# Performance work log

Hardware: AMD Instinct MI355X
Metric: run time of the kernel (lower is better)

The kernel has to match this reference:

```python
import jax, jax.numpy as jnp
import numpy as np

EPS = 1e-5
N_GRAPHS = 64


def gcn_conv(x, W, b, src, dst, n_nodes):
    # GCNConv: out = D^{-1/2} (A + I) D^{-1/2} X W + b
    xw = x @ W  # [N, H]
    # add self loops
    loops = jnp.arange(n_nodes, dtype=src.dtype)
    src_f = jnp.concatenate([src, loops])
    dst_f = jnp.concatenate([dst, loops])
    deg = jax.ops.segment_sum(jnp.ones_like(dst_f, dtype=xw.dtype), dst_f, num_segments=n_nodes)
    dinv = jnp.where(deg > 0, jax.lax.rsqrt(deg), 0.0)
    norm = dinv[src_f] * dinv[dst_f]  # [E+N]
    msg = xw[src_f] * norm[:, None]  # gather + scale
    out = jax.ops.segment_sum(msg, dst_f, num_segments=n_nodes)  # scatter-add
    return out + b


def batchnorm(x):
    # fresh BatchNorm1d in training mode: identity affine, batch stats, biased var
    mean = jnp.mean(x, axis=0)
    var = jnp.mean((x - mean) ** 2, axis=0)
    return (x - mean) * jax.lax.rsqrt(var + EPS)


def setup_inputs() -> dict:
    key = jax.random.key(0)
    ks = jax.random.split(key, 12)
    N, E, F, H, C = 65536, 1048576, 64, 64, 16
    x = jax.random.normal(ks[0], (N, F), dtype=jnp.float32)
    edge_index = jax.random.randint(ks[1], (2, E), 0, N, dtype=jnp.int64)
    batch = jnp.sort(jax.random.randint(ks[2], (N,), 0, N_GRAPHS, dtype=jnp.int64))
    s = 1.0 / np.sqrt(H)
    W0 = jax.random.normal(ks[3], (F, H), dtype=jnp.float32) * s
    b0 = jax.random.normal(ks[4], (H,), dtype=jnp.float32) * 0.1
    W1 = jax.random.normal(ks[5], (H, H), dtype=jnp.float32) * s
    b1 = jax.random.normal(ks[6], (H,), dtype=jnp.float32) * 0.1
    W2 = jax.random.normal(ks[7], (H, H), dtype=jnp.float32) * s
    b2 = jax.random.normal(ks[8], (H,), dtype=jnp.float32) * 0.1
    clf_W = jax.random.normal(ks[9], (C, H), dtype=jnp.float32) * s
    clf_b = jax.random.normal(ks[10], (C,), dtype=jnp.float32) * 0.1
    return {"x": x, "edge_index": edge_index, "batch": batch,
            "W0": W0, "b0": b0, "W1": W1, "b1": b1, "W2": W2, "b2": b2,
            "clf_W": clf_W, "clf_b": clf_b}


def reference(x, edge_index, batch, W0, b0, W1, b1, W2, b2, clf_W, clf_b):
    n_nodes = x.shape[0]
    src, dst = edge_index[0], edge_index[1]
    weights = [(W0, b0), (W1, b1), (W2, b2)]
    n_conv = len(weights)
    h = x
    for i, (W, b) in enumerate(weights):
        h = gcn_conv(h, W, b, src, dst, n_nodes)
        if i < n_conv - 1:
            h = jax.nn.relu(h)
        h = batchnorm(h)
    # global mean pool over graphs
    sums = jax.ops.segment_sum(h, batch, num_segments=N_GRAPHS)
    cnts = jax.ops.segment_sum(jnp.ones((n_nodes,), h.dtype), batch, num_segments=N_GRAPHS)
    pooled = sums / jnp.maximum(cnts, 1.0)[:, None]
    logits = pooled @ clf_W.T + clf_b
    return jax.nn.softmax(logits, axis=1)
```

## Files before the change

### kernel.cpp

```cpp
#include <hip/hip_runtime.h>
#include <hip/hip_fp16.h>


#define NBKT 512
#define CAP  4096
#define BSTRIDE 16
#define NSLOT 16
#define GSL   2048

__device__ inline unsigned pack2h(float a, float b) {
    __half ha = __float2half_rn(a), hb = __float2half_rn(b);
    unsigned short ua = *(unsigned short*)&ha, ub = *(unsigned short*)&hb;
    return (unsigned)ua | ((unsigned)ub << 16);
}

__device__ inline void acc8(float* a, uint4 u) {
    __half2* hp = (__half2*)&u;
#pragma unroll
    for (int i = 0; i < 4; ++i) {
        float2 f = __half22float2(hp[i]);
        a[2 * i] += f.x;
        a[2 * i + 1] += f.y;
    }
}

__global__ void k_binit(int* __restrict__ bcur, float* __restrict__ gstats,
                        float* __restrict__ psum, float* __restrict__ pcnt) {
    int idx = blockIdx.x * 256 + threadIdx.x;
    if (idx < NBKT) bcur[idx * BSTRIDE] = idx * CAP;
    for (int i = idx; i < 3 * NSLOT * GSL; i += 32768) gstats[i] = 0.0f;
    if (idx < 4096) psum[idx] = 0.0f;
    if (idx < 64) pcnt[idx] = 0.0f;
}

__global__ void k_bin(const int* __restrict__ ei, int E, int* __restrict__ bcur,
                      int* __restrict__ buck) {
    __shared__ int sd[4096];
    __shared__ unsigned short bk[4096];
    __shared__ int cnt[NBKT], off[NBKT];
    int t = threadIdx.x;
    int base = blockIdx.x * 4096;
    for (int i = t; i < NBKT; i += 256) cnt[i] = 0;
    __syncthreads();
#pragma unroll
    for (int k = 0; k < 16; ++k) {
        int i = k * 256 + t;
        int e = base + i;
        int s = ei[e], d = ei[E + e];
        sd[i] = (s << 7) | (d & 127);
        int b = d >> 7;
        bk[i] = (unsigned short)b;
        atomicAdd(&cnt[b], 1);
    }
    __syncthreads();
    for (int b = t; b < NBKT; b += 256) {
        int c = cnt[b];
        off[b] = c ? atomicAdd(&bcur[b * BSTRIDE], c) : 0;
    }
    __syncthreads();
#pragma unroll
    for (int k = 0; k < 16; ++k) {
        int i = k * 256 + t;
        int b = bk[i];
        int p = atomicAdd(&off[b], 1);
        buck[p] = sd[i];
    }
}

__global__ void k_scanB(const int* __restrict__ bcur, int* __restrict__ bbase,
                        int* __restrict__ rowptr, int N, int E) {
    __shared__ int s[NBKT];
    int t = threadIdx.x;
    int v = bcur[t * BSTRIDE] - t * CAP;
    s[t] = v;
    __syncthreads();
    for (int o = 1; o < NBKT; o <<= 1) {
        int x = (t >= o) ? s[t - o] : 0;
        __syncthreads();
        s[t] += x;
        __syncthreads();
    }
    bbase[t] = s[t] - v;
    if (t == 0) rowptr[N] = E;
}

__global__ void k_place(const int* __restrict__ bcur, const int* __restrict__ buck,
                        const int* __restrict__ bbase, int* __restrict__ rowptr,
                        float* __restrict__ dinv, int* __restrict__ csr) {
    __shared__ int dc[128], sc[128], cur[128];
    int b = blockIdx.x, t = threadIdx.x;
    if (t < 128) dc[t] = 0;
    __syncthreads();
    int beg = b * CAP, end = bcur[b * BSTRIDE];
    for (int i = beg + t; i < end; i += 256) atomicAdd(&dc[buck[i] & 127], 1);
    __syncthreads();
    int v = (t < 128) ? dc[t] : 0;
    if (t < 128) sc[t] = v;
    __syncthreads();
    for (int o = 1; o < 128; o <<= 1) {
        int x = 0;
        if (t < 128 && t >= o) x = sc[t - o];
        __syncthreads();
        if (t < 128) sc[t] += x;
        __syncthreads();
    }
    if (t < 128) {
        int r = bbase[b] + sc[t] - v;
        rowptr[b * 128 + t] = r;
        cur[t] = r;
        dinv[b * 128 + t] = rsqrtf((float)(v + 1));
    }
    __syncthreads();
    for (int i = beg + t; i < end; i += 256) {
        int e = buck[i];
        int p = atomicAdd(&cur[e & 127], 1);
        csr[p] = e >> 7;
    }
}

template <int HIN, int HS>
__global__ void k_gemm(const void* __restrict__ hv, const float* __restrict__ W,
                       const float* __restrict__ gstats, float invN,
                       const float* __restrict__ dinv, __half* __restrict__ y) {
    __shared__ float Ws[4096];
    __shared__ float hs[64 * 65];
    __shared__ float sm[64], sr[64], bs[64];
    int t = threadIdx.x;
    int rowBase = blockIdx.x * 64;
    if (t < 64) {
        if (HS) {
            float S = 0.0f, Q = 0.0f;
#pragma unroll
            for (int c = 0; c < NSLOT; ++c) {
                S += gstats[c * GSL + t * 16];
                Q += gstats[c * GSL + (64 + t) * 16];
            }
            float m = S * invN;
            float var = Q * invN - m * m;
            sm[t] = m;
            sr[t] = rsqrtf(var + 1e-5f);
        } else {
            sm[t] = 0.0f;
            sr[t] = 1.0f;
        }
    }
    __syncthreads();
#pragma unroll
    for (int k = 0; k < 4; ++k) {
        int i = t + k * 256;
        float4 wv = ((const float4*)W)[i];
        float s = sr[i >> 4];
        wv.x *= s; wv.y *= s; wv.z *= s; wv.w *= s;
        ((float4*)Ws)[i] = wv;
    }
    if (HIN) {
        const uint4* src = (const uint4*)((const __half*)hv + (size_t)rowBase * 64);
#pragma unroll
        for (int k = 0; k < 2; ++k) {
            int i = t + k * 256;
            int row = i >> 3, c8 = i & 7;
            uint4 u = src[i];
            const __half2* hp = (const __half2*)&u;
            float* dst = &hs[row * 65 + c8 * 8];
#pragma unroll
            for (int j = 0; j < 4; ++j) {
                dst[2 * j + 0] = __low2float(hp[j]);
                dst[2 * j + 1] = __high2float(hp[j]);
            }
        }
    } else {
        const float4* src = (const float4*)((const float*)hv + (size_t)rowBase * 64);
#pragma unroll
        for (int k = 0; k < 4; ++k) {
            int i = t + k * 256;
            int row = i >> 4, c4 = i & 15;
            float4 v = src[i];
            float* dst = &hs[row * 65 + c4 * 4];
            dst[0] = v.x; dst[1] = v.y; dst[2] = v.z; dst[3] = v.w;
        }
    }
    __syncthreads();
    if (t < 64) {
        float acc = 0.0f;
        for (int f = 0; f < 64; ++f) acc += sm[f] * Ws[f * 64 + t];
        bs[t] = -acc;
    }
    __syncthreads();
    int rg = t >> 4;
    int cg = t & 15;
    float4 a0, a1, a2, a3;
    {
        float bx = bs[cg * 4 + 0], by = bs[cg * 4 + 1];
        float bz = bs[cg * 4 + 2], bw = bs[cg * 4 + 3];
        a0 = {bx, by, bz, bw}; a1 = a0; a2 = a0; a3 = a0;
    }
    const float* h0 = &hs[(rg * 4 + 0) * 65];
    const float* h1 = &hs[(rg * 4 + 1) * 65];
    const float* h2 = &hs[(rg * 4 + 2) * 65];
    const float* h3 = &hs[(rg * 4 + 3) * 65];
#pragma unroll 4
    for (int f = 0; f < 64; ++f) {
        float4 wv = ((float4*)Ws)[f * 16 + cg];
        float v0 = h0[f], v1 = h1[f], v2 = h2[f], v3 = h3[f];
        a0.x += v0 * wv.x; a0.y += v0 * wv.y; a0.z += v0 * wv.z; a0.w += v0 * wv.w;
        a1.x += v1 * wv.x; a1.y += v1 * wv.y; a1.z += v1 * wv.z; a1.w += v1 * wv.w;
        a2.x += v2 * wv.x; a2.y += v2 * wv.y; a2.z += v2 * wv.z; a2.w += v2 * wv.w;
        a3.x += v3 * wv.x; a3.y += v3 * wv.y; a3.z += v3 * wv.z; a3.w += v3 * wv.w;
    }
    float d0 = dinv[rowBase + rg * 4 + 0];
    float d1 = dinv[rowBase + rg * 4 + 1];
    float d2 = dinv[rowBase + rg * 4 + 2];
    float d3 = dinv[rowBase + rg * 4 + 3];
    uint2* y2 = (uint2*)y;
    size_t ob = (size_t)(rowBase + rg * 4) * 16 + cg;
    y2[ob + 0]  = {pack2h(a0.x * d0, a0.y * d0), pack2h(a0.z * d0, a0.w * d0)};
    y2[ob + 16] = {pack2h(a1.x * d1, a1.y * d1), pack2h(a1.z * d1, a1.w * d1)};
    y2[ob + 32] = {pack2h(a2.x * d2, a2.y * d2), pack2h(a2.z * d2, a2.w * d2)};
    y2[ob + 48] = {pack2h(a3.x * d3, a3.y * d3), pack2h(a3.z * d3, a3.w * d3)};
}

template <int RELU>
__global__ __launch_bounds__(512) void k_agg(
        const __half* __restrict__ y, const int* __restrict__ rowptr,
        const int* __restrict__ csr, const float* __restrict__ dinv,
        const float* __restrict__ bias, __half* __restrict__ hout,
        float* __restrict__ gstats, int N) {
    __shared__ int lcsr[2048];
    __shared__ int lrp[65];
    __shared__ float SW[16][64];
    int t = threadIdx.x;
    int lane = t & 63, wid = t >> 6;
    int o = lane >> 3, j = lane & 7;
    int nodeBase = blockIdx.x * 64;
    if (t < 65) lrp[t] = rowptr[nodeBase + t];
    __syncthreads();
    int wbase = lrp[0];
    int wlen = lrp[64] - wbase;
    bool fits = (wlen <= 2048);
    if (fits)
        for (int i = t; i < wlen; i += 512) lcsr[i] = csr[wbase + i];
    __syncthreads();

    int n = nodeBase + wid * 8 + o;
    int beg = lrp[wid * 8 + o] - wbase;
    int d = lrp[wid * 8 + o + 1] - wbase - beg;
    const uint4* y4 = (const uint4*)y;
    float a[8] = {0, 0, 0, 0, 0, 0, 0, 0};

    if (fits) {
        const int* cp = lcsr + beg;
        int k = 0;
        for (; k + 4 <= d; k += 4) {
            int s0 = cp[k], s1 = cp[k + 1], s2 = cp[k + 2], s3 = cp[k + 3];
            uint4 u0 = y4[(size_t)s0 * 8 + j];
            uint4 u1 = y4[(size_t)s1 * 8 + j];
            uint4 u2 = y4[(size_t)s2 * 8 + j];
            uint4 u3 = y4[(size_t)s3 * 8 + j];
            acc8(a, u0); acc8(a, u1); acc8(a, u2); acc8(a, u3);
        }
        for (; k < d; ++k) {
            uint4 u0 = y4[(size_t)cp[k] * 8 + j];
            acc8(a, u0);
        }
    } else {
        const int* cp = csr + wbase + beg;
        int k = 0;
        for (; k + 4 <= d; k += 4) {
            int s0 = cp[k], s1 = cp[k + 1], s2 = cp[k + 2], s3 = cp[k + 3];
            uint4 u0 = y4[(size_t)s0 * 8 + j];
            uint4 u1 = y4[(size_t)s1 * 8 + j];
            uint4 u2 = y4[(size_t)s2 * 8 + j];
            uint4 u3 = y4[(size_t)s3 * 8 + j];
            acc8(a, u0); acc8(a, u1); acc8(a, u2); acc8(a, u3);
        }
        for (; k < d; ++k) {
            uint4 u0 = y4[(size_t)cp[k] * 8 + j];
            acc8(a, u0);
        }
    }
    uint4 us = y4[(size_t)n * 8 + j];
    acc8(a, us);

    float dv = dinv[n];
    const float4* b4 = (const float4*)bias;
    float4 blo = b4[j * 2], bhi = b4[j * 2 + 1];
    float v[8];
    v[0] = a[0] * dv + blo.x; v[1] = a[1] * dv + blo.y;
    v[2] = a[2] * dv + blo.z; v[3] = a[3] * dv + blo.w;
    v[4] = a[4] * dv + bhi.x; v[5] = a[5] * dv + bhi.y;
    v[6] = a[6] * dv + bhi.z; v[7] = a[7] * dv + bhi.w;
    if (RELU) {
#pragma unroll
        for (int i = 0; i < 8; ++i) v[i] = fmaxf(v[i], 0.0f);
    }
    uint4 ov;
    ov.x = pack2h(v[0], v[1]); ov.y = pack2h(v[2], v[3]);
    ov.z = pack2h(v[4], v[5]); ov.w = pack2h(v[6], v[7]);
    ((uint4*)hout)[(size_t)n * 8 + j] = ov;

    float q[8];
#pragma unroll
    for (int i = 0; i < 8; ++i) q[i] = v[i] * v[i];
#pragma unroll
    for (int st = 8; st <= 32; st <<= 1) {
#pragma unroll
        for (int i = 0; i < 8; ++i) {
            v[i] += __shfl_xor(v[i], st);
            q[i] += __shfl_xor(q[i], st);
        }
    }
    if (o == 0) {
#pragma unroll
        for (int i = 0; i < 8; ++i) {
            SW[wid][j * 8 + i] = v[i];
            SW[8 + wid][j * 8 + i] = q[i];
        }
    }
    __syncthreads();
    if (t < 64) {
        float s = 0.0f, qq = 0.0f;
#pragma unroll
        for (int w = 0; w < 8; ++w) {
            s += SW[w][t];
            qq += SW[8 + w][t];
        }
        float* gs = gstats + (blockIdx.x & (NSLOT - 1)) * GSL;
        atomicAdd(&gs[t * 16], s);
        atomicAdd(&gs[(64 + t) * 16], qq);
    }
}

__global__ void k_pool(const __half* __restrict__ h, const int* __restrict__ batch,
                       const float* __restrict__ gstats, float invN,
                       float* __restrict__ psum, float* __restrict__ pcnt) {
    int lane = threadIdx.x;
    int base = blockIdx.x * 64;
    float S = 0.0f, Q = 0.0f;
#pragma unroll
    for (int c = 0; c < NSLOT; ++c) {
        S += gstats[c * GSL + lane * 16];
        Q += gstats[c * GSL + (64 + lane) * 16];
    }
    float m = S * invN;
    float r = rsqrtf(Q * invN - m * m + 1e-5f);
    int cur = batch[base];
    float acc = 0.0f;
    int runlen = 0;
    for (int i = 0; i < 64; ++i) {
        int n = base + i;
        int g = batch[n];
        if (g != cur) {
            atomicAdd(&psum[cur * 64 + lane], acc);
            if (lane == 0) atomicAdd(&pcnt[cur], (float)runlen);
            acc = 0.0f;
            runlen = 0;
            cur = g;
        }
        acc += (__half2float(h[(size_t)n * 64 + lane]) - m) * r;
        runlen++;
    }
    atomicAdd(&psum[cur * 64 + lane], acc);
    if (lane == 0) atomicAdd(&pcnt[cur], (float)runlen);
}

__global__ void k_head(const float* __restrict__ psum, const float* __restrict__ pcnt,
                       const float* __restrict__ clfW, const float* __restrict__ clfb,
                       float* __restrict__ out) {
    __shared__ float ps[64 * 64];
    __shared__ float wl[16 * 64];
    __shared__ float ci[64];
    int t = threadIdx.x;
    ((float4*)ps)[t] = ((const float4*)psum)[t];
    if (t < 256) ((float4*)wl)[t] = ((const float4*)clfW)[t];
    if (t < 64) ci[t] = 1.0f / fmaxf(pcnt[t], 1.0f);
    __syncthreads();
    int g = t >> 4, c = t & 15;
    float acc = 0.0f;
#pragma unroll 8
    for (int f = 0; f < 64; ++f) acc += ps[g * 64 + f] * wl[c * 64 + f];
    acc = acc * ci[g] + clfb[c];
    float mx = acc;
    for (int o = 1; o < 16; o <<= 1) mx = fmaxf(mx, __shfl_xor(mx, o, 16));
    float e = __expf(acc - mx);
    float s = e;
    for (int o = 1; o < 16; o <<= 1) s += __shfl_xor(s, o, 16);
    out[t] = e / s;
}

extern "C" void kernel_launch(void* const* d_in, const int* in_sizes, int n_in,
                              void* d_out, int out_size, void* d_ws, size_t ws_size,
                              hipStream_t stream) {
    const float* x    = (const float*)d_in[0];
    const int*   ei   = (const int*)d_in[1];
    const int*   bat  = (const int*)d_in[2];
    const float* W0   = (const float*)d_in[3];
    const float* b0   = (const float*)d_in[4];
    const float* W1   = (const float*)d_in[5];
    const float* b1   = (const float*)d_in[6];
    const float* W2   = (const float*)d_in[7];
    const float* b2   = (const float*)d_in[8];
    const float* clfW = (const float*)d_in[9];
    const float* clfb = (const float*)d_in[10];
    float* out = (float*)d_out;

    const int N = in_sizes[0] / 64;
    const int E = in_sizes[1] / 2;
    const int AB = N / 64;

    char* w = (char*)d_ws;
    size_t off = 0;
    auto take = [&](size_t bytes) -> void* {
        off = (off + 255) & ~(size_t)255;
        void* p = w + off;
        off += bytes;
        return p;
    };
    int*    rowptr   = (int*)take((size_t)(N + 1) * 4);
    int*    bcur     = (int*)take((size_t)NBKT * BSTRIDE * 4);
    int*    bbase    = (int*)take((size_t)NBKT * 4);
    float*  dinv     = (float*)take((size_t)N * 4);
    int*    csr      = (int*)take((size_t)E * 4);
    __half* y        = (__half*)take((size_t)N * 64 * 2);
    __half* hA       = (__half*)take((size_t)N * 64 * 2);
    __half* hB       = (__half*)take((size_t)N * 64 * 2);
    float*  gstats   = (float*)take((size_t)3 * NSLOT * GSL * 4);
    float*  psum     = (float*)take(64 * 64 * 4);
    float*  pcnt     = (float*)take(64 * 4);
    int* buck = (int*)hB;
    float* gs0 = gstats;
    float* gs1 = gstats + NSLOT * GSL;
    float* gs2 = gstats + 2 * NSLOT * GSL;

    const float invN = 1.0f / (float)N;

    k_binit<<<128, 256, 0, stream>>>(bcur, gstats, psum, pcnt);
    k_bin<<<E / 4096, 256, 0, stream>>>(ei, E, bcur, buck);
    k_scanB<<<1, NBKT, 0, stream>>>(bcur, bbase, rowptr, N, E);
    k_place<<<NBKT, 256, 0, stream>>>(bcur, buck, bbase, rowptr, dinv, csr);

    k_gemm<0, 0><<<N / 64, 256, 0, stream>>>(x, W0, nullptr, invN, dinv, y);
    k_agg<1><<<AB, 512, 0, stream>>>(y, rowptr, csr, dinv, b0, hA, gs0, N);
    k_gemm<1, 1><<<N / 64, 256, 0, stream>>>(hA, W1, gs0, invN, dinv, y);
    k_agg<1><<<AB, 512, 0, stream>>>(y, rowptr, csr, dinv, b1, hB, gs1, N);
    k_gemm<1, 1><<<N / 64, 256, 0, stream>>>(hB, W2, gs1, invN, dinv, y);
    k_agg<0><<<AB, 512, 0, stream>>>(y, rowptr, csr, dinv, b2, hA, gs2, N);

    k_pool<<<N / 64, 64, 0, stream>>>(hA, bat, gs2, invN, psum, pcnt);
    k_head<<<1, 1024, 0, stream>>>(psum, pcnt, clfW, clfb, out);
}
```

Before: 192.3 us.

## Fuse bucket scan into place kernel and pool+head into per-graph kernel

```diff
diff --git a/kernel.cpp b/kernel.cpp
--- a/kernel.cpp
+++ b/kernel.cpp
@@ -24,13 +24,10 @@
     }
 }
 
-__global__ void k_binit(int* __restrict__ bcur, float* __restrict__ gstats,
-                        float* __restrict__ psum, float* __restrict__ pcnt) {
+__global__ void k_binit(int* __restrict__ bcur, float* __restrict__ gstats) {
     int idx = blockIdx.x * 256 + threadIdx.x;
     if (idx < NBKT) bcur[idx * BSTRIDE] = idx * CAP;
     for (int i = idx; i < 3 * NSLOT * GSL; i += 32768) gstats[i] = 0.0f;
-    if (idx < 4096) psum[idx] = 0.0f;
-    if (idx < 64) pcnt[idx] = 0.0f;
 }
 
 __global__ void k_bin(const int* __restrict__ ei, int E, int* __restrict__ bcur,
@@ -67,12 +64,16 @@
     }
 }
 
-__global__ void k_scanB(const int* __restrict__ bcur, int* __restrict__ bbase,
-                        int* __restrict__ rowptr, int N, int E) {
+__global__ __launch_bounds__(512) void k_place(
+        const int* __restrict__ bcur, const int* __restrict__ buck,
+        int* __restrict__ rowptr, float* __restrict__ dinv, int* __restrict__ csr,
+        int N, int E) {
     __shared__ int s[NBKT];
-    int t = threadIdx.x;
-    int v = bcur[t * BSTRIDE] - t * CAP;
-    s[t] = v;
+    __shared__ int dc[128], sc[128], cur[128];
+    __shared__ int sbase;
+    int b = blockIdx.x, t = threadIdx.x;
+    s[t] = bcur[t * BSTRIDE] - t * CAP;
+    if (t < 128) dc[t] = 0;
     __syncthreads();
     for (int o = 1; o < NBKT; o <<= 1) {
         int x = (t >= o) ? s[t - o] : 0;
@@ -80,19 +81,13 @@
         s[t] += x;
         __syncthreads();
     }
-    bbase[t] = s[t] - v;
-    if (t == 0) rowptr[N] = E;
-}
-
-__global__ void k_place(const int* __restrict__ bcur, const int* __restrict__ buck,
-                        const int* __restrict__ bbase, int* __restrict__ rowptr,
-                        float* __restrict__ dinv, int* __restrict__ csr) {
-    __shared__ int dc[128], sc[128], cur[128];
-    int b = blockIdx.x, t = threadIdx.x;
-    if (t < 128) dc[t] = 0;
+    if (t == 0) {
+        sbase = (b == 0) ? 0 : s[b - 1];
+        if (b == NBKT - 1) rowptr[N] = E;
+    }
     __syncthreads();
     int beg = b * CAP, end = bcur[b * BSTRIDE];
-    for (int i = beg + t; i < end; i += 256) atomicAdd(&dc[buck[i] & 127], 1);
+    for (int i = beg + t; i < end; i += 512) atomicAdd(&dc[buck[i] & 127], 1);
     __syncthreads();
     int v = (t < 128) ? dc[t] : 0;
     if (t < 128) sc[t] = v;
@@ -105,13 +100,13 @@
         __syncthreads();
     }
     if (t < 128) {
-        int r = bbase[b] + sc[t] - v;
+        int r = sbase + sc[t] - v;
         rowptr[b * 128 + t] = r;
         cur[t] = r;
         dinv[b * 128 + t] = rsqrtf((float)(v + 1));
     }
     __syncthreads();
-    for (int i = beg + t; i < end; i += 256) {
+    for (int i = beg + t; i < end; i += 512) {
         int e = buck[i];
         int p = atomicAdd(&cur[e & 127], 1);
         csr[p] = e >> 7;
@@ -330,11 +325,25 @@
     }
 }
 
-__global__ void k_pool(const __half* __restrict__ h, const int* __restrict__ batch,
-                       const float* __restrict__ gstats, float invN,
-                       float* __restrict__ psum, float* __restrict__ pcnt) {
-    int lane = threadIdx.x;
-    int base = blockIdx.x * 64;
+__global__ __launch_bounds__(512) void k_poolhead(
+        const __half* __restrict__ h, const int* __restrict__ batch,
+        const float* __restrict__ gstats, float invN,
+        const float* __restrict__ clfW, const float* __restrict__ clfb,
+        float* __restrict__ out, int N) {
+    __shared__ float SWm[8][64];
+    __shared__ float pooled[64];
+    __shared__ int rng[2];
+    int g = blockIdx.x;
+    int t = threadIdx.x;
+    int lane = t & 63, wid = t >> 6;
+    if (t < 2) {
+        int key = g + t, lo = 0, hi = N;
+        while (lo < hi) {
+            int mid = (lo + hi) >> 1;
+            if (batch[mid] < key) lo = mid + 1; else hi = mid;
+        }
+        rng[t] = lo;
+    }
     float S = 0.0f, Q = 0.0f;
 #pragma unroll
     for (int c = 0; c < NSLOT; ++c) {
@@ -343,48 +352,34 @@
     }
     float m = S * invN;
     float r = rsqrtf(Q * invN - m * m + 1e-5f);
-    int cur = batch[base];
+    __syncthreads();
+    int lo = rng[0], hi = rng[1];
     float acc = 0.0f;
-    int runlen = 0;
-    for (int i = 0; i < 64; ++i) {
-        int n = base + i;
-        int g = batch[n];
-        if (g != cur) {
-            atomicAdd(&psum[cur * 64 + lane], acc);
-            if (lane == 0) atomicAdd(&pcnt[cur], (float)runlen);
-            acc = 0.0f;
-            runlen = 0;
-            cur = g;
-        }
+    for (int n = lo + wid; n < hi; n += 8)
         acc += (__half2float(h[(size_t)n * 64 + lane]) - m) * r;
-        runlen++;
-    }
-    atomicAdd(&psum[cur * 64 + lane], acc);
-    if (lane == 0) atomicAdd(&pcnt[cur], (float)runlen);
-}
-
-__global__ void k_head(const float* __restrict__ psum, const float* __restrict__ pcnt,
-                       const float* __restrict__ clfW, const float* __restrict__ clfb,
-                       float* __restrict__ out) {
-    __shared__ float ps[64 * 64];
-    __shared__ float wl[16 * 64];
-    __shared__ float ci[64];
-    int t = threadIdx.x;
-    ((float4*)ps)[t] = ((const float4*)psum)[t];
-    if (t < 256) ((float4*)wl)[t] = ((const float4*)clfW)[t];
-    if (t < 64) ci[t] = 1.0f / fmaxf(pcnt[t], 1.0f);
-    __syncthreads();
-    int g = t >> 4, c = t & 15;
-    float acc = 0.0f;
+    SWm[wid][lane] = acc;
+    __syncthreads();
+    if (t < 64) {
+        float s = 0.0f;
+#pragma unroll
+        for (int w = 0; w < 8; ++w) s += SWm[w][t];
+        pooled[t] = s / fmaxf((float)(hi - lo), 1.0f);
+    }
+    __syncthreads();
+    if (t < 16) {
+        float a = 0.0f;
 #pragma unroll 8
-    for (int f = 0; f < 64; ++f) acc += ps[g * 64 + f] * wl[c * 64 + f];
-    acc = acc * ci[g] + clfb[c];
-    float mx = acc;
-    for (int o = 1; o < 16; o <<= 1) mx = fmaxf(mx, __shfl_xor(mx, o, 16));
-    float e = __expf(acc - mx);
-    float s = e;
-    for (int o = 1; o < 16; o <<= 1) s += __shfl_xor(s, o, 16);
-    out[t] = e / s;
+        for (int f = 0; f < 64; ++f) a += pooled[f] * clfW[t * 64 + f];
+        a += clfb[t];
+        float mx = a;
+#pragma unroll
+        for (int o = 1; o < 16; o <<= 1) mx = fmaxf(mx, __shfl_xor(mx, o, 16));
+        float e = __expf(a - mx);
+        float sum = e;
+#pragma unroll
+        for (int o = 1; o < 16; o <<= 1) sum += __shfl_xor(sum, o, 16);
+        out[g * 16 + t] = e / sum;
+    }
 }
 
 extern "C" void kernel_launch(void* const* d_in, const int* in_sizes, int n_in,
@@ -417,15 +412,12 @@
     };
     int*    rowptr   = (int*)take((size_t)(N + 1) * 4);
     int*    bcur     = (int*)take((size_t)NBKT * BSTRIDE * 4);
-    int*    bbase    = (int*)take((size_t)NBKT * 4);
     float*  dinv     = (float*)take((size_t)N * 4);
     int*    csr      = (int*)take((size_t)E * 4);
     __half* y        = (__half*)take((size_t)N * 64 * 2);
     __half* hA       = (__half*)take((size_t)N * 64 * 2);
     __half* hB       = (__half*)take((size_t)N * 64 * 2);
     float*  gstats   = (float*)take((size_t)3 * NSLOT * GSL * 4);
-    float*  psum     = (float*)take(64 * 64 * 4);
-    float*  pcnt     = (float*)take(64 * 4);
     int* buck = (int*)hB;
     float* gs0 = gstats;
     float* gs1 = gstats + NSLOT * GSL;
@@ -433,10 +425,9 @@
 
     const float invN = 1.0f / (float)N;
 
-    k_binit<<<128, 256, 0, stream>>>(bcur, gstats, psum, pcnt);
+    k_binit<<<128, 256, 0, stream>>>(bcur, gstats);
     k_bin<<<E / 4096, 256, 0, stream>>>(ei, E, bcur, buck);
-    k_scanB<<<1, NBKT, 0, stream>>>(bcur, bbase, rowptr, N, E);
-    k_place<<<NBKT, 256, 0, stream>>>(bcur, buck, bbase, rowptr, dinv, csr);
+    k_place<<<NBKT, 512, 0, stream>>>(bcur, buck, rowptr, dinv, csr, N, E);
 
     k_gemm<0, 0><<<N / 64, 256, 0, stream>>>(x, W0, nullptr, invN, dinv, y);
     k_agg<1><<<AB, 512, 0, stream>>>(y, rowptr, csr, dinv, b0, hA, gs0, N);
@@ -445,6 +436,5 @@
     k_gemm<1, 1><<<N / 64, 256, 0, stream>>>(hB, W2, gs1, invN, dinv, y);
     k_agg<0><<<AB, 512, 0, stream>>>(y, rowptr, csr, dinv, b2, hA, gs2, N);
 
-    k_pool<<<N / 64, 64, 0, stream>>>(hA, bat, gs2, invN, psum, pcnt);
-    k_head<<<1, 1024, 0, stream>>>(psum, pcnt, clfW, clfb, out);
-}
+    k_poolhead<<<64, 512, 0, stream>>>(hA, bat, gs2, invN, clfW, clfb, out, N);
+}
```

New measurement: 199.4 us. 1.04x slower.
